# Kernel optimization log

Hardware: AMD Instinct MI355X
Metric: run time of the kernel (lower is better)

## Reference

```python
import jax, jax.numpy as jnp
import numpy as np

B, N, D_POINTS, D_MODEL = 2, 2048, 32, 512


def _gather(feat, idx):
    # feat: [B, N, C], idx: [B, N, K] -> [B, N, K, C]
    return jax.vmap(lambda f, i: f[i])(feat, idx)


def setup_inputs() -> dict:
    key = jax.random.key(0)
    ks = jax.random.split(key, 20)
    def lin(k, fan_in, fan_out):
        bound = 1.0 / np.sqrt(fan_in)
        return jax.random.uniform(k, (fan_in, fan_out), jnp.float32, -bound, bound)
    def bias(k, fan_in, fan_out):
        bound = 1.0 / np.sqrt(fan_in)
        return jax.random.uniform(k, (fan_out,), jnp.float32, -bound, bound)
    return {
        "xyz": jax.random.normal(ks[0], (B, N, 3), jnp.float32),
        "points": jax.random.normal(ks[1], (B, N, D_POINTS), jnp.float32),
        "fc1_w": lin(ks[2], D_POINTS, D_MODEL), "fc1_b": bias(ks[3], D_POINTS, D_MODEL),
        "fc2_w": lin(ks[4], D_MODEL, D_POINTS), "fc2_b": bias(ks[5], D_MODEL, D_POINTS),
        "delta_w1": lin(ks[6], 3, D_MODEL), "delta_b1": bias(ks[7], 3, D_MODEL),
        "delta_w2": lin(ks[8], D_MODEL, D_MODEL), "delta_b2": bias(ks[9], D_MODEL, D_MODEL),
        "gamma_w1": lin(ks[10], D_MODEL, D_MODEL), "gamma_b1": bias(ks[11], D_MODEL, D_MODEL),
        "gamma_w2": lin(ks[12], D_MODEL, D_MODEL), "gamma_b2": bias(ks[13], D_MODEL, D_MODEL),
        "wq": lin(ks[14], D_MODEL, D_MODEL),
        "wk": lin(ks[15], D_MODEL, D_MODEL),
        "wv": lin(ks[16], D_MODEL, D_MODEL),
        "knn_k": 16,
    }


def reference(xyz, points, fc1_w, fc1_b, fc2_w, fc2_b,
              delta_w1, delta_b1, delta_w2, delta_b2,
              gamma_w1, gamma_b1, gamma_w2, gamma_b2,
              wq, wk, wv, knn_k):
    # square_distance: [B, N, N]
    sq = jnp.sum(xyz * xyz, axis=-1)
    dists = sq[:, :, None] + sq[:, None, :] - 2.0 * jnp.einsum('bnc,bmc->bnm', xyz, xyz)
    # knn: k smallest distances (argsort[:, :, :k] equivalent)
    _, knn_idx = jax.lax.top_k(-dists, knn_k)           # [B, N, K]
    knn_xyz = _gather(xyz, knn_idx)                      # [B, N, K, 3]

    pre = points
    x = points @ fc1_w + fc1_b                           # [B, N, d_model]
    q = x @ wq                                           # [B, N, d_model]
    k = _gather(x @ wk, knn_idx)                         # [B, N, K, d_model]
    v = _gather(x @ wv, knn_idx)                         # [B, N, K, d_model]

    # positional encoding MLP on delta xyz
    delta = xyz[:, :, None, :] - knn_xyz                 # [B, N, K, 3]
    pos_enc = jax.nn.relu(delta @ delta_w1 + delta_b1) @ delta_w2 + delta_b2

    # gamma MLP on (q - k + pos_enc)
    a = q[:, :, None, :] - k + pos_enc
    a = jax.nn.relu(a @ gamma_w1 + gamma_b1) @ gamma_w2 + gamma_b2

    scale = jnp.asarray(np.sqrt(D_MODEL), a.dtype)
    attn = jax.nn.softmax(a / scale, axis=-2)            # softmax over neighbors, per channel

    res = jnp.sum(attn * (v + pos_enc), axis=2)          # einsum 'bmnf,bmnf->bmf'
    res = res @ fc2_w + fc2_b + pre                      # [B, N, d_points]
    return res, attn
```

## Files before the change

### kernel.cpp

```cpp
#include <hip/hip_runtime.h>
#include <hip/hip_bf16.h>
#include <math.h>

typedef __bf16 bf16_t;
typedef float f32x4 __attribute__((ext_vector_type(4)));
typedef bf16_t bf16x8 __attribute__((ext_vector_type(8)));

#define BM 128
#define BN 128
#define BKT 64

#define GLD_LDS16(gp, lp) __builtin_amdgcn_global_load_lds( \
    (const __attribute__((address_space(1))) void*)(gp), \
    (__attribute__((address_space(3))) void*)(lp), 16, 0, 0)

struct TC7 { const float* src[7]; bf16_t* dst[7]; };
__global__ __launch_bounds__(256) void tcast7_kernel(TC7 tc) {
  int job = blockIdx.x >> 10;
  int idx = (blockIdx.x & 1023) * 256 + threadIdx.x;
  if (job < 6) {
    int n = idx >> 9, k = idx & 511;
    tc.dst[job][idx] = (bf16_t)tc.src[job][k * 512 + n];
  } else {
    tc.dst[job][idx] = (bf16_t)tc.src[job][idx];
  }
}

__global__ __launch_bounds__(256) void cc_kernel(const float* __restrict__ db2, const float* __restrict__ gw1,
                                                 const float* __restrict__ gb1, float* __restrict__ cc) {
  int n = blockIdx.x * 256 + threadIdx.x;
  float s = gb1[n];
  for (int d = 0; d < 512; ++d) s = fmaf(db2[d], gw1[d * 512 + n], s);
  cc[n] = s;
}

__global__ __launch_bounds__(256) void knn_kernel(const float* __restrict__ xyz, int* __restrict__ knn) {
  __shared__ float sx[2048], sy[2048], sz[2048], sq[2048];
  int tid = threadIdx.x;
  int lane = tid & 63, wave = tid >> 6;
  int gq = blockIdx.x * 4 + wave;
  int b  = gq >> 11;
  int base = b << 11;
  for (int p = tid; p < 2048; p += 256) {
    float x = xyz[(base + p) * 3 + 0];
    float y = xyz[(base + p) * 3 + 1];
    float z = xyz[(base + p) * 3 + 2];
    sx[p] = x; sy[p] = y; sz[p] = z;
    sq[p] = __fadd_rn(__fadd_rn(__fmul_rn(x, x), __fmul_rn(y, y)), __fmul_rn(z, z));
  }
  __syncthreads();
  int iq = gq & 2047;
  float qx = sx[iq], qy = sy[iq], qz = sz[iq], sqi = sq[iq];

  unsigned long long key[32];
  #pragma unroll
  for (int j = 0; j < 32; ++j) {
    int p = lane + j * 64;
    float d = __fmul_rn(sx[p], qx);
    d = fmaf(sy[p], qy, d);
    d = fmaf(sz[p], qz, d);
    float dist = __fsub_rn(__fadd_rn(sqi, sq[p]), __fmul_rn(2.0f, d));
    unsigned int bits = __float_as_uint(dist);
    unsigned int sk = bits ^ (unsigned int)(((int)bits >> 31) | 0x80000000);
    key[j] = ((unsigned long long)sk << 32) | (unsigned int)p;
  }

  int r = 0;
  #pragma unroll 1
  for (int s = 0; s < 16; ++s) {
    unsigned long long m = key[0];
    #pragma unroll
    for (int j = 1; j < 32; ++j) m = (key[j] < m) ? key[j] : m;
    #pragma unroll
    for (int off = 32; off > 0; off >>= 1) {
      unsigned long long o = (unsigned long long)__shfl_xor((long long)m, off);
      if (o < m) m = o;
    }
    if (lane == s) r = base + (int)(m & 0xFFFFFFFFu);
    #pragma unroll
    for (int j = 0; j < 32; ++j) key[j] = (key[j] == m) ? ~0ULL : key[j];
  }
  if (lane < 16) knn[gq * 16 + lane] = r;
}

__global__ __launch_bounds__(256) void xfeat_kernel(const float* __restrict__ points, const float* __restrict__ fc1_w,
                                                    const float* __restrict__ fc1_b, bf16_t* __restrict__ xb) {
  __shared__ float p[32];
  int m = blockIdx.x, tid = threadIdx.x;
  if (tid < 32) p[tid] = points[m * 32 + tid];
  __syncthreads();
  for (int c = tid; c < 512; c += 256) {
    float a = fc1_b[c];
    #pragma unroll
    for (int kk = 0; kk < 32; ++kk) a = fmaf(p[kk], fc1_w[kk * 512 + c], a);
    xb[m * 512 + c] = (bf16_t)a;
  }
}

__global__ __launch_bounds__(256) void final_kernel(const float* __restrict__ res_mid, const float* __restrict__ fc2_w,
                                                    const float* __restrict__ fc2_b, const float* __restrict__ points,
                                                    float* __restrict__ out) {
  int oid = blockIdx.x * 256 + threadIdx.x;
  int m = oid >> 5, c = oid & 31;
  float a = fc2_b[c];
  const float* rm = res_mid + m * 512;
  for (int kk = 0; kk < 512; ++kk) a = fmaf(rm[kk], fc2_w[kk * 32 + c], a);
  out[oid] = a + points[oid];
}

struct GP {
  const bf16_t* A; const bf16_t* Bt; const bf16_t* Bt2;
  bf16_t* Cb; const float* bias; int ldc;
  const float* xyz; const int* knn; const float* dw1; const float* db1;
  const float* cc; const bf16_t* qkg; float* pe; bf16_t* h2;
  const bf16_t* vb; float* pe_attn; float* res_mid;
};

template <int SRC, int EPI>
__global__ __launch_bounds__(256) void gemm_kernel(GP gp) {
  __shared__ bf16_t Alds[BM * BKT];
  __shared__ bf16_t Blds[BN * BKT];
  __shared__ bf16_t B2lds[(EPI == 5) ? (BN * BKT) : 8];
  int tid  = threadIdx.x;
  int lane = tid & 63, wave = tid >> 6;
  int wr = wave >> 1, wc = wave & 1;
  int lr = lane & 15, lg = lane >> 4;

  int gx = gridDim.x;
  int nwg = gx * gridDim.y;
  int orig = blockIdx.y * gx + blockIdx.x;
  int cpx = nwg >> 3;
  int swz = (orig & 7) * cpx + (orig >> 3);
  int bx = swz % gx;
  int by = swz / gx;
  int n0 = bx * BN, m0 = by * BM;

  f32x4 acc[4][4];
  f32x4 acc2[4][4];
  #pragma unroll
  for (int i = 0; i < 4; ++i)
    #pragma unroll
    for (int j = 0; j < 4; ++j) {
      acc[i][j] = (f32x4){0.f, 0.f, 0.f, 0.f};
      if (EPI == 5) acc2[i][j] = (f32x4){0.f, 0.f, 0.f, 0.f};
    }

  int rS  = tid >> 3;
  int sc8 = (tid & 7) << 3;
  int scS = (((tid & 7) ^ ((tid >> 3) & 7)) << 3);

  float dx[4], dy[4], dz[4];
  if (SRC == 2) {
    #pragma unroll
    for (int it = 0; it < 4; ++it) {
      int m = m0 + it * 32 + rS;
      int g = m >> 4;
      int j = gp.knn[m];
      dx[it] = gp.xyz[g * 3 + 0] - gp.xyz[j * 3 + 0];
      dy[it] = gp.xyz[g * 3 + 1] - gp.xyz[j * 3 + 1];
      dz[it] = gp.xyz[g * 3 + 2] - gp.xyz[j * 3 + 2];
    }
  }

  #pragma unroll 1
  for (int k0 = 0; k0 < 512; k0 += BKT) {
    if (SRC == 0) {
      #pragma unroll
      for (int it = 0; it < 4; ++it)
        GLD_LDS16(gp.A + (size_t)(m0 + it * 32 + rS) * 512 + k0 + scS, Alds + (it * 4 + wave) * 512);
    } else {
      const float* w0p = gp.dw1 + k0 + sc8;
      f32x4 w0a = *(const f32x4*)w0p,          w0b = *(const f32x4*)(w0p + 4);
      f32x4 w1a = *(const f32x4*)(w0p + 512),  w1b = *(const f32x4*)(w0p + 516);
      f32x4 w2a = *(const f32x4*)(w0p + 1024), w2b = *(const f32x4*)(w0p + 1028);
      const float* bbp = gp.db1 + k0 + sc8;
      f32x4 bba = *(const f32x4*)bbp,          bbb = *(const f32x4*)(bbp + 4);
      #pragma unroll
      for (int it = 0; it < 4; ++it) {
        bf16x8 o;
        #pragma unroll
        for (int u = 0; u < 4; ++u) {
          float h = fmaf(dz[it], w2a[u], fmaf(dy[it], w1a[u], dx[it] * w0a[u])) + bba[u];
          o[u] = (bf16_t)fmaxf(h, 0.0f);
        }
        #pragma unroll
        for (int u = 0; u < 4; ++u) {
          float h = fmaf(dz[it], w2b[u], fmaf(dy[it], w1b[u], dx[it] * w0b[u])) + bbb[u];
          o[4 + u] = (bf16_t)fmaxf(h, 0.0f);
        }
        *(bf16x8*)(&Alds[(it * 32 + rS) * BKT + scS]) = o;
      }
    }
    #pragma unroll
    for (int it = 0; it < 4; ++it)
      GLD_LDS16(gp.Bt + (size_t)(n0 + it * 32 + rS) * 512 + k0 + scS, Blds + (it * 4 + wave) * 512);
    if (EPI == 5) {
      #pragma unroll
      for (int it = 0; it < 4; ++it)
        GLD_LDS16(gp.Bt2 + (size_t)(n0 + it * 32 + rS) * 512 + k0 + scS, B2lds + (it * 4 + wave) * 512);
    }
    __syncthreads();

    #pragma unroll
    for (int kk = 0; kk < BKT; kk += 32) {
      int ks = (kk >> 3) + lg;
      bf16x8 af[4], bfr[4], b2r[4];
      #pragma unroll
      for (int mi = 0; mi < 4; ++mi) {
        int rr = wr * 64 + mi * 16 + lr;
        af[mi] = *(const bf16x8*)(&Alds[rr * BKT + ((ks ^ (rr & 7)) << 3)]);
      }
      #pragma unroll
      for (int nj = 0; nj < 4; ++nj) {
        int rr = wc * 64 + nj * 16 + lr;
        bfr[nj] = *(const bf16x8*)(&Blds[rr * BKT + ((ks ^ (rr & 7)) << 3)]);
        if (EPI == 5) b2r[nj] = *(const bf16x8*)(&B2lds[rr * BKT + ((ks ^ (rr & 7)) << 3)]);
      }
      #pragma unroll
      for (int mi = 0; mi < 4; ++mi)
        #pragma unroll
        for (int nj = 0; nj < 4; ++nj) {
          acc[mi][nj] = __builtin_amdgcn_mfma_f32_16x16x32_bf16(af[mi], bfr[nj], acc[mi][nj], 0, 0, 0);
          if (EPI == 5)
            acc2[mi][nj] = __builtin_amdgcn_mfma_f32_16x16x32_bf16(af[mi], b2r[nj], acc2[mi][nj], 0, 0, 0);
        }
    }
    __syncthreads();
  }

  if (EPI == 4) {
    #pragma unroll
    for (int mi = 0; mi < 4; ++mi)
      #pragma unroll
      for (int nj = 0; nj < 4; ++nj) {
        int col = n0 + wc * 64 + nj * 16 + lr;
        #pragma unroll
        for (int r = 0; r < 4; ++r) {
          int row = m0 + wr * 64 + mi * 16 + lg * 4 + r;
          gp.Cb[(size_t)col * 512 + row] = (bf16_t)acc[mi][nj][r];
        }
      }
  } else if (EPI == 6) {
    #pragma unroll
    for (int mi = 0; mi < 4; ++mi)
      #pragma unroll
      for (int nj = 0; nj < 4; ++nj) {
        int col = n0 + wc * 64 + nj * 16 + lr;
        int part = col >> 9, c = col & 511;
        #pragma unroll
        for (int r = 0; r < 4; ++r) {
          int row = m0 + wr * 64 + mi * 16 + lg * 4 + r;
          gp.Cb[((size_t)part * 4096 + row) * 512 + c] = (bf16_t)acc[mi][nj][r];
        }
      }
  } else if (EPI == 7) {
    #pragma unroll
    for (int mi = 0; mi < 4; ++mi)
      #pragma unroll
      for (int nj = 0; nj < 4; ++nj) {
        int col = n0 + wc * 64 + nj * 16 + lr;
        #pragma unroll
        for (int r = 0; r < 4; ++r) {
          int row = m0 + wr * 64 + mi * 16 + lg * 4 + r;
          gp.Cb[(size_t)row * gp.ldc + col] = (bf16_t)acc[mi][nj][r];
        }
      }
  } else if (EPI == 5) {
    #pragma unroll
    for (int mi = 0; mi < 4; ++mi) {
      int g = (m0 + wr * 64 + mi * 16) >> 4;
      #pragma unroll
      for (int nj = 0; nj < 4; ++nj) {
        int col = n0 + wc * 64 + nj * 16 + lr;
        float db2v = gp.bias[col];
        float ccv  = gp.cc[col];
        float qgv  = (float)gp.qkg[(size_t)g * 512 + col];
        #pragma unroll
        for (int r = 0; r < 4; ++r) {
          int row = m0 + wr * 64 + mi * 16 + lg * 4 + r;
          gp.pe[(size_t)row * 512 + col] = acc[mi][nj][r] + db2v;
          int j = gp.knn[row];
          float kgv = (float)gp.qkg[(size_t)(4096 + j) * 512 + col];
          float hv = acc2[mi][nj][r] + ccv + qgv - kgv;
          gp.h2[(size_t)row * 512 + col] = (bf16_t)fmaxf(hv, 0.0f);
        }
      }
    }
  } else {
    const float scale = 22.62741699796952f;
    #pragma unroll
    for (int mi = 0; mi < 4; ++mi) {
      int g = (m0 + wr * 64 + mi * 16) >> 4;
      #pragma unroll
      for (int nj = 0; nj < 4; ++nj) {
        int col = n0 + wc * 64 + nj * 16 + lr;
        float sv[4];
        float mx = -INFINITY;
        #pragma unroll
        for (int r = 0; r < 4; ++r) {
          sv[r] = (acc[mi][nj][r] + gp.bias[col]) / scale;
          mx = fmaxf(mx, sv[r]);
        }
        mx = fmaxf(mx, __shfl_xor(mx, 16));
        mx = fmaxf(mx, __shfl_xor(mx, 32));
        float e[4], sum = 0.f;
        #pragma unroll
        for (int r = 0; r < 4; ++r) { e[r] = expf(sv[r] - mx); sum += e[r]; }
        sum += __shfl_xor(sum, 16);
        sum += __shfl_xor(sum, 32);
        float part = 0.f;
        #pragma unroll
        for (int r = 0; r < 4; ++r) {
          int row = g * 16 + lg * 4 + r;
          float at = e[r] / sum;
          int j = gp.knn[row];
          float vv  = (float)gp.vb[(size_t)j * 512 + col];
          float pev = gp.pe_attn[(size_t)row * 512 + col];
          part = fmaf(at, vv + pev, part);
          gp.pe_attn[(size_t)row * 512 + col] = at;
        }
        part += __shfl_xor(part, 16);
        part += __shfl_xor(part, 32);
        if (lg == 0) gp.res_mid[(size_t)g * 512 + col] = part;
      }
    }
  }
}

extern "C" void kernel_launch(void* const* d_in, const int* in_sizes, int n_in,
                              void* d_out, int out_size, void* d_ws, size_t ws_size,
                              hipStream_t stream) {
  const float* xyz    = (const float*)d_in[0];
  const float* points = (const float*)d_in[1];
  const float* fc1_w  = (const float*)d_in[2];
  const float* fc1_b  = (const float*)d_in[3];
  const float* fc2_w  = (const float*)d_in[4];
  const float* fc2_b  = (const float*)d_in[5];
  const float* dw1    = (const float*)d_in[6];
  const float* db1    = (const float*)d_in[7];
  const float* dw2    = (const float*)d_in[8];
  const float* db2    = (const float*)d_in[9];
  const float* gw1    = (const float*)d_in[10];
  const float* gb1    = (const float*)d_in[11];
  const float* gw2    = (const float*)d_in[12];
  const float* gb2    = (const float*)d_in[13];
  const float* wq     = (const float*)d_in[14];
  const float* wk     = (const float*)d_in[15];
  const float* wv     = (const float*)d_in[16];

  float* out = (float*)d_out;
  float* attn_pe = out + 131072;

  char* w = (char*)d_ws;
  bf16_t* wqkvT  = (bf16_t*)w; w += (size_t)1536 * 512 * 2;
  bf16_t* dw2T   = (bf16_t*)w; w += (size_t)512 * 512 * 2;
  bf16_t* gw1T   = (bf16_t*)w; w += (size_t)512 * 512 * 2;
  bf16_t* gw2T   = (bf16_t*)w; w += (size_t)512 * 512 * 2;
  bf16_t* dw2b   = (bf16_t*)w; w += (size_t)512 * 512 * 2;
  bf16_t* WpT    = (bf16_t*)w; w += (size_t)512 * 512 * 2;
  float*  cc     = (float*)w;  w += (size_t)512 * 4;
  int*    knn    = (int*)w;    w += (size_t)65536 * 4;
  bf16_t* xb     = (bf16_t*)w; w += (size_t)4096 * 512 * 2;
  bf16_t* qkvb   = (bf16_t*)w; w += (size_t)3 * 4096 * 512 * 2;
  bf16_t* qkg    = (bf16_t*)w; w += (size_t)2 * 4096 * 512 * 2;
  bf16_t* h2     = (bf16_t*)w; w += (size_t)65536 * 512 * 2;
  float*  res_mid= (float*)w;  w += (size_t)4096 * 512 * 4;

  TC7 tc;
  tc.src[0] = wq;  tc.dst[0] = wqkvT;
  tc.src[1] = wk;  tc.dst[1] = wqkvT + 512 * 512;
  tc.src[2] = wv;  tc.dst[2] = wqkvT + 2 * 512 * 512;
  tc.src[3] = dw2; tc.dst[3] = dw2T;
  tc.src[4] = gw1; tc.dst[4] = gw1T;
  tc.src[5] = gw2; tc.dst[5] = gw2T;
  tc.src[6] = dw2; tc.dst[6] = dw2b;
  tcast7_kernel<<<7168, 256, 0, stream>>>(tc);

  knn_kernel<<<1024, 256, 0, stream>>>(xyz, knn);
  xfeat_kernel<<<4096, 256, 0, stream>>>(points, fc1_w, fc1_b, xb);
  cc_kernel<<<2, 256, 0, stream>>>(db2, gw1, gb1, cc);

  GP gp{};
  gp.A = dw2b; gp.Bt = gw1T; gp.Cb = WpT; gp.ldc = 512;
  gemm_kernel<0, 4><<<dim3(4, 4), 256, 0, stream>>>(gp);

  GP gq{};
  gq.A = xb; gq.Bt = wqkvT; gq.Cb = qkvb; gq.ldc = 1536;
  gemm_kernel<0, 6><<<dim3(12, 32), 256, 0, stream>>>(gq);

  GP gk{};
  gk.A = qkvb; gk.Bt = gw1T; gk.Cb = qkg; gk.ldc = 512;
  gemm_kernel<0, 7><<<dim3(4, 64), 256, 0, stream>>>(gk);

  GP gd{};
  gd.Bt = dw2T; gd.Bt2 = WpT; gd.bias = db2;
  gd.xyz = xyz; gd.knn = knn; gd.dw1 = dw1; gd.db1 = db1;
  gd.cc = cc; gd.qkg = qkg; gd.pe = attn_pe; gd.h2 = h2;
  gemm_kernel<2, 5><<<dim3(4, 512), 256, 0, stream>>>(gd);

  GP gs{};
  gs.A = h2; gs.Bt = gw2T; gs.bias = gb2;
  gs.knn = knn; gs.vb = qkvb + (size_t)2 * 4096 * 512; gs.pe_attn = attn_pe; gs.res_mid = res_mid;
  gemm_kernel<0, 3><<<dim3(4, 512), 256, 0, stream>>>(gs);

  final_kernel<<<512, 256, 0, stream>>>(res_mid, fc2_w, fc2_b, points, out);
}
```

Baseline: 514.4 us.

## Double-buffer GEMM LDS tiles and split dual-output pos-enc GEMM into two kernels

Switches the shared GEMM kernel to a two-stage LDS ping-pong, issuing the next K-tile's global-to-LDS loads before computing the current one. The wait is manual s_waitcnt plus raw s_barrier instead of __syncthreads. The fused pos-enc/gamma kernel that used two B matrices and two accumulator sets is split into two launches (EPI 1 writes pos_enc, EPI 2 writes h2). This lowers register and LDS pressure per kernel, at the cost of recomputing the delta MLP A tile twice and launching an extra kernel.

```diff
diff --git a/kernel.cpp b/kernel.cpp
--- a/kernel.cpp
+++ b/kernel.cpp
@@ -109,18 +109,17 @@
 }
 
 struct GP {
-  const bf16_t* A; const bf16_t* Bt; const bf16_t* Bt2;
-  bf16_t* Cb; const float* bias; int ldc;
+  const bf16_t* A; const bf16_t* Bt;
+  bf16_t* Cb; float* Cf; const float* bias; int ldc;
   const float* xyz; const int* knn; const float* dw1; const float* db1;
-  const float* cc; const bf16_t* qkg; float* pe; bf16_t* h2;
+  const float* cc; const bf16_t* qkg;
   const bf16_t* vb; float* pe_attn; float* res_mid;
 };
 
 template <int SRC, int EPI>
 __global__ __launch_bounds__(256) void gemm_kernel(GP gp) {
-  __shared__ bf16_t Alds[BM * BKT];
-  __shared__ bf16_t Blds[BN * BKT];
-  __shared__ bf16_t B2lds[(EPI == 5) ? (BN * BKT) : 8];
+  __shared__ bf16_t Alds[2 * BM * BKT];
+  __shared__ bf16_t Blds[2 * BN * BKT];
   int tid  = threadIdx.x;
   int lane = tid & 63, wave = tid >> 6;
   int wr = wave >> 1, wc = wave & 1;
@@ -136,14 +135,10 @@
   int n0 = bx * BN, m0 = by * BM;
 
   f32x4 acc[4][4];
-  f32x4 acc2[4][4];
   #pragma unroll
   for (int i = 0; i < 4; ++i)
     #pragma unroll
-    for (int j = 0; j < 4; ++j) {
-      acc[i][j] = (f32x4){0.f, 0.f, 0.f, 0.f};
-      if (EPI == 5) acc2[i][j] = (f32x4){0.f, 0.f, 0.f, 0.f};
-    }
+    for (int j = 0; j < 4; ++j) acc[i][j] = (f32x4){0.f, 0.f, 0.f, 0.f};
 
   int rS  = tid >> 3;
   int sc8 = (tid & 7) << 3;
@@ -162,12 +157,13 @@
     }
   }
 
-  #pragma unroll 1
-  for (int k0 = 0; k0 < 512; k0 += BKT) {
+  auto stageA = [&](int t, int buf) {
+    int k0 = t * BKT;
     if (SRC == 0) {
       #pragma unroll
       for (int it = 0; it < 4; ++it)
-        GLD_LDS16(gp.A + (size_t)(m0 + it * 32 + rS) * 512 + k0 + scS, Alds + (it * 4 + wave) * 512);
+        GLD_LDS16(gp.A + (size_t)(m0 + it * 32 + rS) * 512 + k0 + scS,
+                  Alds + buf * (BM * BKT) + (it * 4 + wave) * 512);
     } else {
       const float* w0p = gp.dw1 + k0 + sc8;
       f32x4 w0a = *(const f32x4*)w0p,          w0b = *(const f32x4*)(w0p + 4);
@@ -175,6 +171,7 @@
       f32x4 w2a = *(const f32x4*)(w0p + 1024), w2b = *(const f32x4*)(w0p + 1028);
       const float* bbp = gp.db1 + k0 + sc8;
       f32x4 bba = *(const f32x4*)bbp,          bbb = *(const f32x4*)(bbp + 4);
+      bf16_t* Ab = Alds + buf * (BM * BKT);
       #pragma unroll
       for (int it = 0; it < 4; ++it) {
         bf16x8 o;
@@ -188,47 +185,92 @@
           float h = fmaf(dz[it], w2b[u], fmaf(dy[it], w1b[u], dx[it] * w0b[u])) + bbb[u];
           o[4 + u] = (bf16_t)fmaxf(h, 0.0f);
         }
-        *(bf16x8*)(&Alds[(it * 32 + rS) * BKT + scS]) = o;
-      }
-    }
+        *(bf16x8*)(&Ab[(it * 32 + rS) * BKT + scS]) = o;
+      }
+    }
+  };
+  auto stageB = [&](int t, int buf) {
+    int k0 = t * BKT;
     #pragma unroll
     for (int it = 0; it < 4; ++it)
-      GLD_LDS16(gp.Bt + (size_t)(n0 + it * 32 + rS) * 512 + k0 + scS, Blds + (it * 4 + wave) * 512);
-    if (EPI == 5) {
-      #pragma unroll
-      for (int it = 0; it < 4; ++it)
-        GLD_LDS16(gp.Bt2 + (size_t)(n0 + it * 32 + rS) * 512 + k0 + scS, B2lds + (it * 4 + wave) * 512);
-    }
-    __syncthreads();
-
+      GLD_LDS16(gp.Bt + (size_t)(n0 + it * 32 + rS) * 512 + k0 + scS,
+                Blds + buf * (BN * BKT) + (it * 4 + wave) * 512);
+  };
+
+  const int NT = 8;
+  stageA(0, 0);
+  stageB(0, 0);
+
+  #pragma unroll 1
+  for (int t = 0; t < NT; ++t) {
+    int cur = t & 1;
+    if (t + 1 < NT) {
+      stageA(t + 1, cur ^ 1);
+      stageB(t + 1, cur ^ 1);
+      if (SRC == 0) asm volatile("s_waitcnt vmcnt(8)" ::: "memory");
+      else          asm volatile("s_waitcnt vmcnt(4) lgkmcnt(0)" ::: "memory");
+    } else {
+      asm volatile("s_waitcnt vmcnt(0) lgkmcnt(0)" ::: "memory");
+    }
+    __builtin_amdgcn_s_barrier();
+
+    const bf16_t* Ab = Alds + cur * (BM * BKT);
+    const bf16_t* Bb = Blds + cur * (BN * BKT);
     #pragma unroll
     for (int kk = 0; kk < BKT; kk += 32) {
       int ks = (kk >> 3) + lg;
-      bf16x8 af[4], bfr[4], b2r[4];
+      bf16x8 af[4], bfr[4];
       #pragma unroll
       for (int mi = 0; mi < 4; ++mi) {
         int rr = wr * 64 + mi * 16 + lr;
-        af[mi] = *(const bf16x8*)(&Alds[rr * BKT + ((ks ^ (rr & 7)) << 3)]);
+        af[mi] = *(const bf16x8*)(&Ab[rr * BKT + ((ks ^ (rr & 7)) << 3)]);
       }
       #pragma unroll
       for (int nj = 0; nj < 4; ++nj) {
         int rr = wc * 64 + nj * 16 + lr;
-        bfr[nj] = *(const bf16x8*)(&Blds[rr * BKT + ((ks ^ (rr & 7)) << 3)]);
-        if (EPI == 5) b2r[nj] = *(const bf16x8*)(&B2lds[rr * BKT + ((ks ^ (rr & 7)) << 3)]);
+        bfr[nj] = *(const bf16x8*)(&Bb[rr * BKT + ((ks ^ (rr & 7)) << 3)]);
       }
       #pragma unroll
       for (int mi = 0; mi < 4; ++mi)
         #pragma unroll
-        for (int nj = 0; nj < 4; ++nj) {
+        for (int nj = 0; nj < 4; ++nj)
           acc[mi][nj] = __builtin_amdgcn_mfma_f32_16x16x32_bf16(af[mi], bfr[nj], acc[mi][nj], 0, 0, 0);
-          if (EPI == 5)
-            acc2[mi][nj] = __builtin_amdgcn_mfma_f32_16x16x32_bf16(af[mi], b2r[nj], acc2[mi][nj], 0, 0, 0);
-        }
-    }
-    __syncthreads();
-  }
-
-  if (EPI == 4) {
+    }
+    __builtin_amdgcn_s_barrier();
+  }
+
+  if (EPI == 1) {
+    #pragma unroll
+    for (int mi = 0; mi < 4; ++mi)
+      #pragma unroll
+      for (int nj = 0; nj < 4; ++nj) {
+        int col = n0 + wc * 64 + nj * 16 + lr;
+        #pragma unroll
+        for (int r = 0; r < 4; ++r) {
+          int row = m0 + wr * 64 + mi * 16 + lg * 4 + r;
+          gp.Cf[(size_t)row * gp.ldc + col] = acc[mi][nj][r] + gp.bias[col];
+        }
+      }
+  } else if (EPI == 2) {
+    #pragma unroll
+    for (int mi = 0; mi < 4; ++mi) {
+      int g = (m0 + wr * 64 + mi * 16) >> 4;
+      #pragma unroll
+      for (int nj = 0; nj < 4; ++nj) {
+        int col = n0 + wc * 64 + nj * 16 + lr;
+        float ccv = gp.cc[col];
+        float qgv = (float)gp.qkg[(size_t)g * 512 + col];
+        #pragma unroll
+        for (int r = 0; r < 4; ++r) {
+          int row = m0 + wr * 64 + mi * 16 + lg * 4 + r;
+          int j = gp.knn[row];
+          float kgv = (float)gp.qkg[(size_t)(4096 + j) * 512 + col];
+          float hv = acc[mi][nj][r] + ccv + qgv - kgv;
+          gp.Cb[(size_t)row * 512 + col] = (bf16_t)fmaxf(hv, 0.0f);
+        }
+      }
+    }
+  } else if (EPI == 4) {
     #pragma unroll
     for (int mi = 0; mi < 4; ++mi)
       #pragma unroll
@@ -265,27 +307,6 @@
           gp.Cb[(size_t)row * gp.ldc + col] = (bf16_t)acc[mi][nj][r];
         }
       }
-  } else if (EPI == 5) {
-    #pragma unroll
-    for (int mi = 0; mi < 4; ++mi) {
-      int g = (m0 + wr * 64 + mi * 16) >> 4;
-      #pragma unroll
-      for (int nj = 0; nj < 4; ++nj) {
-        int col = n0 + wc * 64 + nj * 16 + lr;
-        float db2v = gp.bias[col];
-        float ccv  = gp.cc[col];
-        float qgv  = (float)gp.qkg[(size_t)g * 512 + col];
-        #pragma unroll
-        for (int r = 0; r < 4; ++r) {
-          int row = m0 + wr * 64 + mi * 16 + lg * 4 + r;
-          gp.pe[(size_t)row * 512 + col] = acc[mi][nj][r] + db2v;
-          int j = gp.knn[row];
-          float kgv = (float)gp.qkg[(size_t)(4096 + j) * 512 + col];
-          float hv = acc2[mi][nj][r] + ccv + qgv - kgv;
-          gp.h2[(size_t)row * 512 + col] = (bf16_t)fmaxf(hv, 0.0f);
-        }
-      }
-    }
   } else {
     const float scale = 22.62741699796952f;
     #pragma unroll
@@ -392,11 +413,16 @@
   gk.A = qkvb; gk.Bt = gw1T; gk.Cb = qkg; gk.ldc = 512;
   gemm_kernel<0, 7><<<dim3(4, 64), 256, 0, stream>>>(gk);
 
-  GP gd{};
-  gd.Bt = dw2T; gd.Bt2 = WpT; gd.bias = db2;
-  gd.xyz = xyz; gd.knn = knn; gd.dw1 = dw1; gd.db1 = db1;
-  gd.cc = cc; gd.qkg = qkg; gd.pe = attn_pe; gd.h2 = h2;
-  gemm_kernel<2, 5><<<dim3(4, 512), 256, 0, stream>>>(gd);
+  GP gpe{};
+  gpe.Bt = dw2T; gpe.Cf = attn_pe; gpe.bias = db2; gpe.ldc = 512;
+  gpe.xyz = xyz; gpe.knn = knn; gpe.dw1 = dw1; gpe.db1 = db1;
+  gemm_kernel<2, 1><<<dim3(4, 512), 256, 0, stream>>>(gpe);
+
+  GP gg{};
+  gg.Bt = WpT; gg.Cb = h2;
+  gg.xyz = xyz; gg.knn = knn; gg.dw1 = dw1; gg.db1 = db1;
+  gg.cc = cc; gg.qkg = qkg;
+  gemm_kernel<2, 2><<<dim3(4, 512), 256, 0, stream>>>(gg);
 
   GP gs{};
   gs.A = h2; gs.Bt = gw2T; gs.bias = gb2;
```

New measurement: 473.2 us. -8.0%, faster.

## Double-buffer GEMM LDS tiles with BK=32 and cache pos-MLP weights in LDS

Applied to the files above, without the earlier changes.

The shared GEMM kernel now uses two LDS buffers with a 32-wide K tile. It prefetches the next tile through global_load_lds while MFMAs run on the current one, using manual vmcnt waits and raw s_barrier instead of __syncthreads. For the fused positional-encoding GEMM, the delta MLP first-layer weights and bias are staged once into LDS rather than reread from global memory every K step, and acc2 is sized down for non-dual epilogues. The aim is to hide load latency. The cost is more LDS per block, twice as many loop iterations, and the risk that the hand-written waitcnt counts are wrong.

```diff
diff --git a/kernel.cpp b/kernel.cpp
--- a/kernel.cpp
+++ b/kernel.cpp
@@ -8,7 +8,8 @@
 
 #define BM 128
 #define BN 128
-#define BKT 64
+#define BKT 32
+#define NT 16
 
 #define GLD_LDS16(gp, lp) __builtin_amdgcn_global_load_lds( \
     (const __attribute__((address_space(1))) void*)(gp), \
@@ -110,17 +111,18 @@
 
 struct GP {
   const bf16_t* A; const bf16_t* Bt; const bf16_t* Bt2;
-  bf16_t* Cb; const float* bias; int ldc;
+  bf16_t* Cb; float* Cf; const float* bias; int ldc;
   const float* xyz; const int* knn; const float* dw1; const float* db1;
-  const float* cc; const bf16_t* qkg; float* pe; bf16_t* h2;
+  const float* cc; const bf16_t* qkg;
   const bf16_t* vb; float* pe_attn; float* res_mid;
 };
 
 template <int SRC, int EPI>
 __global__ __launch_bounds__(256) void gemm_kernel(GP gp) {
-  __shared__ bf16_t Alds[BM * BKT];
-  __shared__ bf16_t Blds[BN * BKT];
-  __shared__ bf16_t B2lds[(EPI == 5) ? (BN * BKT) : 8];
+  __shared__ bf16_t Alds[2 * BM * BKT];
+  __shared__ bf16_t Blds[2 * BN * BKT];
+  __shared__ bf16_t B2lds[(EPI == 5) ? (2 * BN * BKT) : 8];
+  __shared__ float  wl[(SRC == 2) ? 4 * 512 : 8];
   int tid  = threadIdx.x;
   int lane = tid & 63, wave = tid >> 6;
   int wr = wave >> 1, wc = wave & 1;
@@ -136,7 +138,7 @@
   int n0 = bx * BN, m0 = by * BM;
 
   f32x4 acc[4][4];
-  f32x4 acc2[4][4];
+  f32x4 acc2[(EPI == 5) ? 4 : 1][4];
   #pragma unroll
   for (int i = 0; i < 4; ++i)
     #pragma unroll
@@ -145,87 +147,123 @@
       if (EPI == 5) acc2[i][j] = (f32x4){0.f, 0.f, 0.f, 0.f};
     }
 
-  int rS  = tid >> 3;
-  int sc8 = (tid & 7) << 3;
-  int scS = (((tid & 7) ^ ((tid >> 3) & 7)) << 3);
-
-  float dx[4], dy[4], dz[4];
+  int rS2 = tid >> 2;
+  int sl  = tid & 3;
+  int swb = (rS2 >> 1) & 3;
+  int scS = ((sl ^ swb) << 3);
+
+  float dx0, dy0, dz0, dx1, dy1, dz1;
   if (SRC == 2) {
-    #pragma unroll
-    for (int it = 0; it < 4; ++it) {
-      int m = m0 + it * 32 + rS;
-      int g = m >> 4;
-      int j = gp.knn[m];
-      dx[it] = gp.xyz[g * 3 + 0] - gp.xyz[j * 3 + 0];
-      dy[it] = gp.xyz[g * 3 + 1] - gp.xyz[j * 3 + 1];
-      dz[it] = gp.xyz[g * 3 + 2] - gp.xyz[j * 3 + 2];
-    }
-  }
+    for (int c = tid; c < 512; c += 256) {
+      wl[c]        = gp.dw1[c];
+      wl[512 + c]  = gp.dw1[512 + c];
+      wl[1024 + c] = gp.dw1[1024 + c];
+      wl[1536 + c] = gp.db1[c];
+    }
+    int m_a = m0 + rS2, m_b = m0 + rS2 + 64;
+    int ga = m_a >> 4, ja = gp.knn[m_a];
+    int gb = m_b >> 4, jb = gp.knn[m_b];
+    dx0 = gp.xyz[ga * 3 + 0] - gp.xyz[ja * 3 + 0];
+    dy0 = gp.xyz[ga * 3 + 1] - gp.xyz[ja * 3 + 1];
+    dz0 = gp.xyz[ga * 3 + 2] - gp.xyz[ja * 3 + 2];
+    dx1 = gp.xyz[gb * 3 + 0] - gp.xyz[jb * 3 + 0];
+    dy1 = gp.xyz[gb * 3 + 1] - gp.xyz[jb * 3 + 1];
+    dz1 = gp.xyz[gb * 3 + 2] - gp.xyz[jb * 3 + 2];
+    __syncthreads();
+  }
+
+  auto stageA = [&](int t, int buf) {
+    int k0 = t * BKT;
+    if (SRC == 0) {
+      GLD_LDS16(gp.A + (size_t)(m0 + rS2) * 512 + k0 + scS,       Alds + buf * (BM * BKT) + tid * 8);
+      GLD_LDS16(gp.A + (size_t)(m0 + 64 + rS2) * 512 + k0 + scS,  Alds + buf * (BM * BKT) + 2048 + tid * 8);
+    } else {
+      int cb = k0 + sl * 8;
+      f32x4 w0a = *(const f32x4*)(&wl[cb]),        w0b = *(const f32x4*)(&wl[cb + 4]);
+      f32x4 w1a = *(const f32x4*)(&wl[512 + cb]),  w1b = *(const f32x4*)(&wl[512 + cb + 4]);
+      f32x4 w2a = *(const f32x4*)(&wl[1024 + cb]), w2b = *(const f32x4*)(&wl[1024 + cb + 4]);
+      f32x4 bba = *(const f32x4*)(&wl[1536 + cb]), bbb = *(const f32x4*)(&wl[1536 + cb + 4]);
+      bf16_t* Ab = Alds + buf * (BM * BKT);
+      bf16x8 o;
+      #pragma unroll
+      for (int u = 0; u < 4; ++u) {
+        float h = fmaf(dz0, w2a[u], fmaf(dy0, w1a[u], dx0 * w0a[u])) + bba[u];
+        o[u] = (bf16_t)fmaxf(h, 0.0f);
+      }
+      #pragma unroll
+      for (int u = 0; u < 4; ++u) {
+        float h = fmaf(dz0, w2b[u], fmaf(dy0, w1b[u], dx0 * w0b[u])) + bbb[u];
+        o[4 + u] = (bf16_t)fmaxf(h, 0.0f);
+      }
+      *(bf16x8*)(&Ab[rS2 * BKT + ((sl ^ swb) << 3)]) = o;
+      #pragma unroll
+      for (int u = 0; u < 4; ++u) {
+        float h = fmaf(dz1, w2a[u], fmaf(dy1, w1a[u], dx1 * w0a[u])) + bba[u];
+        o[u] = (bf16_t)fmaxf(h, 0.0f);
+      }
+      #pragma unroll
+      for (int u = 0; u < 4; ++u) {
+        float h = fmaf(dz1, w2b[u], fmaf(dy1, w1b[u], dx1 * w0b[u])) + bbb[u];
+        o[4 + u] = (bf16_t)fmaxf(h, 0.0f);
+      }
+      *(bf16x8*)(&Ab[(rS2 + 64) * BKT + ((sl ^ swb) << 3)]) = o;
+    }
+  };
+  auto stageB = [&](int t, int buf) {
+    int k0 = t * BKT;
+    GLD_LDS16(gp.Bt + (size_t)(n0 + rS2) * 512 + k0 + scS,       Blds + buf * (BN * BKT) + tid * 8);
+    GLD_LDS16(gp.Bt + (size_t)(n0 + 64 + rS2) * 512 + k0 + scS,  Blds + buf * (BN * BKT) + 2048 + tid * 8);
+    if (EPI == 5) {
+      GLD_LDS16(gp.Bt2 + (size_t)(n0 + rS2) * 512 + k0 + scS,      B2lds + buf * (BN * BKT) + tid * 8);
+      GLD_LDS16(gp.Bt2 + (size_t)(n0 + 64 + rS2) * 512 + k0 + scS, B2lds + buf * (BN * BKT) + 2048 + tid * 8);
+    }
+  };
+
+  stageA(0, 0);
+  stageB(0, 0);
 
   #pragma unroll 1
-  for (int k0 = 0; k0 < 512; k0 += BKT) {
-    if (SRC == 0) {
-      #pragma unroll
-      for (int it = 0; it < 4; ++it)
-        GLD_LDS16(gp.A + (size_t)(m0 + it * 32 + rS) * 512 + k0 + scS, Alds + (it * 4 + wave) * 512);
+  for (int t = 0; t < NT; ++t) {
+    int cur = t & 1;
+    if (t + 1 < NT) {
+      stageA(t + 1, cur ^ 1);
+      stageB(t + 1, cur ^ 1);
+      if (SRC == 0) {
+        if (EPI == 5) asm volatile("s_waitcnt vmcnt(6)" ::: "memory");
+        else          asm volatile("s_waitcnt vmcnt(4)" ::: "memory");
+      } else {
+        if (EPI == 5) asm volatile("s_waitcnt vmcnt(4) lgkmcnt(0)" ::: "memory");
+        else          asm volatile("s_waitcnt vmcnt(2) lgkmcnt(0)" ::: "memory");
+      }
     } else {
-      const float* w0p = gp.dw1 + k0 + sc8;
-      f32x4 w0a = *(const f32x4*)w0p,          w0b = *(const f32x4*)(w0p + 4);
-      f32x4 w1a = *(const f32x4*)(w0p + 512),  w1b = *(const f32x4*)(w0p + 516);
-      f32x4 w2a = *(const f32x4*)(w0p + 1024), w2b = *(const f32x4*)(w0p + 1028);
-      const float* bbp = gp.db1 + k0 + sc8;
-      f32x4 bba = *(const f32x4*)bbp,          bbb = *(const f32x4*)(bbp + 4);
-      #pragma unroll
-      for (int it = 0; it < 4; ++it) {
-        bf16x8 o;
-        #pragma unroll
-        for (int u = 0; u < 4; ++u) {
-          float h = fmaf(dz[it], w2a[u], fmaf(dy[it], w1a[u], dx[it] * w0a[u])) + bba[u];
-          o[u] = (bf16_t)fmaxf(h, 0.0f);
-        }
-        #pragma unroll
-        for (int u = 0; u < 4; ++u) {
-          float h = fmaf(dz[it], w2b[u], fmaf(dy[it], w1b[u], dx[it] * w0b[u])) + bbb[u];
-          o[4 + u] = (bf16_t)fmaxf(h, 0.0f);
-        }
-        *(bf16x8*)(&Alds[(it * 32 + rS) * BKT + scS]) = o;
-      }
-    }
-    #pragma unroll
-    for (int it = 0; it < 4; ++it)
-      GLD_LDS16(gp.Bt + (size_t)(n0 + it * 32 + rS) * 512 + k0 + scS, Blds + (it * 4 + wave) * 512);
-    if (EPI == 5) {
-      #pragma unroll
-      for (int it = 0; it < 4; ++it)
-        GLD_LDS16(gp.Bt2 + (size_t)(n0 + it * 32 + rS) * 512 + k0 + scS, B2lds + (it * 4 + wave) * 512);
-    }
-    __syncthreads();
-
-    #pragma unroll
-    for (int kk = 0; kk < BKT; kk += 32) {
-      int ks = (kk >> 3) + lg;
-      bf16x8 af[4], bfr[4], b2r[4];
-      #pragma unroll
-      for (int mi = 0; mi < 4; ++mi) {
-        int rr = wr * 64 + mi * 16 + lr;
-        af[mi] = *(const bf16x8*)(&Alds[rr * BKT + ((ks ^ (rr & 7)) << 3)]);
-      }
-      #pragma unroll
-      for (int nj = 0; nj < 4; ++nj) {
-        int rr = wc * 64 + nj * 16 + lr;
-        bfr[nj] = *(const bf16x8*)(&Blds[rr * BKT + ((ks ^ (rr & 7)) << 3)]);
-        if (EPI == 5) b2r[nj] = *(const bf16x8*)(&B2lds[rr * BKT + ((ks ^ (rr & 7)) << 3)]);
-      }
-      #pragma unroll
-      for (int mi = 0; mi < 4; ++mi)
-        #pragma unroll
-        for (int nj = 0; nj < 4; ++nj) {
-          acc[mi][nj] = __builtin_amdgcn_mfma_f32_16x16x32_bf16(af[mi], bfr[nj], acc[mi][nj], 0, 0, 0);
-          if (EPI == 5)
-            acc2[mi][nj] = __builtin_amdgcn_mfma_f32_16x16x32_bf16(af[mi], b2r[nj], acc2[mi][nj], 0, 0, 0);
-        }
-    }
-    __syncthreads();
+      asm volatile("s_waitcnt vmcnt(0) lgkmcnt(0)" ::: "memory");
+    }
+    __builtin_amdgcn_s_barrier();
+
+    const bf16_t* Ab = Alds + cur * (BM * BKT);
+    const bf16_t* Bb = Blds + cur * (BN * BKT);
+    const bf16_t* B2b = B2lds + cur * (BN * BKT);
+    bf16x8 af[4], bfr[4], b2r[4];
+    #pragma unroll
+    for (int mi = 0; mi < 4; ++mi) {
+      int rr = wr * 64 + mi * 16 + lr;
+      af[mi] = *(const bf16x8*)(&Ab[rr * BKT + ((lg ^ ((rr >> 1) & 3)) << 3)]);
+    }
+    #pragma unroll
+    for (int nj = 0; nj < 4; ++nj) {
+      int rr = wc * 64 + nj * 16 + lr;
+      bfr[nj] = *(const bf16x8*)(&Bb[rr * BKT + ((lg ^ ((rr >> 1) & 3)) << 3)]);
+      if (EPI == 5) b2r[nj] = *(const bf16x8*)(&B2b[rr * BKT + ((lg ^ ((rr >> 1) & 3)) << 3)]);
+    }
+    #pragma unroll
+    for (int mi = 0; mi < 4; ++mi)
+      #pragma unroll
+      for (int nj = 0; nj < 4; ++nj) {
+        acc[mi][nj] = __builtin_amdgcn_mfma_f32_16x16x32_bf16(af[mi], bfr[nj], acc[mi][nj], 0, 0, 0);
+        if (EPI == 5)
+          acc2[mi][nj] = __builtin_amdgcn_mfma_f32_16x16x32_bf16(af[mi], b2r[nj], acc2[mi][nj], 0, 0, 0);
+      }
+    __builtin_amdgcn_s_barrier();
   }
 
   if (EPI == 4) {
@@ -278,11 +316,11 @@
         #pragma unroll
         for (int r = 0; r < 4; ++r) {
           int row = m0 + wr * 64 + mi * 16 + lg * 4 + r;
-          gp.pe[(size_t)row * 512 + col] = acc[mi][nj][r] + db2v;
+          gp.Cf[(size_t)row * 512 + col] = acc[mi][nj][r] + db2v;
           int j = gp.knn[row];
           float kgv = (float)gp.qkg[(size_t)(4096 + j) * 512 + col];
           float hv = acc2[mi][nj][r] + ccv + qgv - kgv;
-          gp.h2[(size_t)row * 512 + col] = (bf16_t)fmaxf(hv, 0.0f);
+          gp.Cb[(size_t)row * 512 + col] = (bf16_t)fmaxf(hv, 0.0f);
         }
       }
     }
@@ -393,9 +431,9 @@
   gemm_kernel<0, 7><<<dim3(4, 64), 256, 0, stream>>>(gk);
 
   GP gd{};
-  gd.Bt = dw2T; gd.Bt2 = WpT; gd.bias = db2;
+  gd.Bt = dw2T; gd.Bt2 = WpT; gd.Cf = attn_pe; gd.Cb = h2; gd.bias = db2;
   gd.xyz = xyz; gd.knn = knn; gd.dw1 = dw1; gd.db1 = db1;
-  gd.cc = cc; gd.qkg = qkg; gd.pe = attn_pe; gd.h2 = h2;
+  gd.cc = cc; gd.qkg = qkg;
   gemm_kernel<2, 5><<<dim3(4, 512), 256, 0, stream>>>(gd);
 
   GP gs{};
```

New measurement: 504.9 us. No clear change (-1.9%).
